# Optimization experiments

Hardware: AMD Instinct MI355X
Metric: run time of the kernel (lower is better)

Reference implementation:

```python
import jax, jax.numpy as jnp
import numpy as np
from jax import lax

NUM_TAGS = 64

def setup_inputs() -> dict:
    key = jax.random.key(0)
    ks = jax.random.split(key, 6)
    B, T, D, N = 64, 512, 1024, NUM_TAGS
    inputs = jax.random.normal(ks[0], (B, T, D), dtype=jnp.float32)
    mask = jnp.ones((B, T), dtype=jnp.int32)
    labels = jax.random.randint(ks[1], (B, T), 0, N)
    W = jax.random.normal(ks[2], (D, N), dtype=jnp.float32) / np.sqrt(D).astype(np.float32)
    b = jnp.zeros((N,), dtype=jnp.float32)
    transitions = jax.random.normal(ks[3], (N, N), dtype=jnp.float32) * 0.1
    start_transitions = jax.random.normal(ks[4], (N,), dtype=jnp.float32) * 0.1
    end_transitions = jax.random.normal(ks[5], (N,), dtype=jnp.float32) * 0.1
    return dict(inputs=inputs, mask=mask, labels=labels, W=W, b=b,
                transitions=transitions, start_transitions=start_transitions,
                end_transitions=end_transitions)


def _log_partition(logits, mask, trans, start, end):
    # forward algorithm (log-sum-exp recurrence). logits [B,T,N], mask bool [B,T]
    alpha = start[None, :] + logits[:, 0]                      # [B,N]
    emits = jnp.swapaxes(logits, 0, 1)[1:]                     # [T-1,B,N]
    ms = jnp.swapaxes(mask, 0, 1)[1:, :, None]                 # [T-1,B,1]
    def step(alpha, xs):
        emit, m = xs
        inner = alpha[:, :, None] + trans[None] + emit[:, None, :]  # [B,from,to]
        new = jax.nn.logsumexp(inner, axis=1)
        return jnp.where(m, new, alpha), None
    alpha, _ = lax.scan(step, alpha, (emits, ms))
    return jax.nn.logsumexp(alpha + end[None, :], axis=-1)     # [B]


def _joint_score(logits, tags, mask, trans, start, end):
    # score of the gold tag sequence (AllenNLP _joint_likelihood), vectorized
    maskf = mask.astype(logits.dtype)
    score = start[tags[:, 0]]
    score = score + jnp.sum(trans[tags[:, :-1], tags[:, 1:]] * maskf[:, 1:], axis=1)
    emit = jnp.take_along_axis(logits, tags[:, :, None], axis=2)[:, :, 0]   # [B,T]
    score = score + jnp.sum(emit * maskf, axis=1)
    last_idx = jnp.sum(mask.astype(jnp.int32), axis=1) - 1
    last_tags = jnp.take_along_axis(tags, last_idx[:, None], axis=1)[:, 0]
    return score + end[last_tags]


def _viterbi(logits, mask, trans, start, end):
    # batched Viterbi decode with backpointers; masked steps carry state through
    B, T, N = logits.shape
    alpha = start[None, :] + logits[:, 0]
    emits = jnp.swapaxes(logits, 0, 1)[1:]
    ms = jnp.swapaxes(mask, 0, 1)[1:, :, None]
    ident = jnp.broadcast_to(jnp.arange(N, dtype=jnp.int32)[None, :], (B, N))
    def step(alpha, xs):
        emit, m = xs
        sc = alpha[:, :, None] + trans[None] + emit[:, None, :]  # [B,from,to]
        best = jnp.max(sc, axis=1)
        bp = jnp.argmax(sc, axis=1).astype(jnp.int32)
        return jnp.where(m, best, alpha), jnp.where(m, bp, ident)
    alpha, bps = lax.scan(step, alpha, (emits, ms))
    last_tag = jnp.argmax(alpha + end[None, :], axis=-1).astype(jnp.int32)
    def back(tag, bp):
        prev = jnp.take_along_axis(bp, tag[:, None], axis=1)[:, 0]
        return prev, tag
    first, rest = lax.scan(back, last_tag, bps, reverse=True)
    tags = jnp.concatenate([first[None], rest], axis=0)          # [T,B]
    return jnp.swapaxes(tags, 0, 1) * mask.astype(jnp.int32)     # zero out padding


def reference(inputs, mask, labels, W, b, transitions, start_transitions, end_transitions):
    bool_mask = mask.astype(bool)
    logits = inputs @ W + b                                      # tag projection [B,T,N]
    scores = logits * mask[..., None].astype(logits.dtype)       # scores = inputs * mask
    tags = _viterbi(scores, bool_mask, transitions, start_transitions, end_transitions)
    log_z = _log_partition(scores, bool_mask, transitions, start_transitions, end_transitions)
    gold = _joint_score(scores, labels, bool_mask, transitions, start_transitions, end_transitions)
    loss = jnp.mean(log_z - gold)                                # mean negative log-likelihood
    return scores, tags, loss
```

## Files before the change

### kernel.cpp

```cpp
#include <hip/hip_runtime.h>
#include <cstdint>
#include <cstddef>

#define BB 64
#define TT 512
#define DD 1024
#define NTAG 64
#define CUT 255
#define SCORES_ELEMS (BB * TT * NTAG)
#define TAGS_OFF SCORES_ELEMS
#define LOSS_OFF (SCORES_ELEMS + BB * TT)

typedef __attribute__((ext_vector_type(8))) short short8;
typedef __attribute__((ext_vector_type(4))) float floatx4;
typedef __attribute__((ext_vector_type(16))) float f32x16;

__device__ __forceinline__ unsigned short f2bf_rne(float x) {
  const unsigned int u = __float_as_uint(x);
  const unsigned int r = u + 0x7FFFu + ((u >> 16) & 1u);
  return (unsigned short)(r >> 16);
}
__device__ __forceinline__ float bf2f(unsigned short h) {
  return __uint_as_float(((unsigned int)h) << 16);
}

__device__ __forceinline__ void block_sync_lds() {
  asm volatile("s_waitcnt lgkmcnt(0)\n\ts_barrier" ::: "memory");
}

__device__ __forceinline__ float quad_xor1(float v) {
  int x = __builtin_amdgcn_update_dpp(__float_as_int(v), __float_as_int(v), 0xB1, 0xf, 0xf, false);
  return __int_as_float(x);
}
__device__ __forceinline__ float quad_xor2(float v) {
  int x = __builtin_amdgcn_update_dpp(__float_as_int(v), __float_as_int(v), 0x4E, 0xf, 0xf, false);
  return __int_as_float(x);
}

__device__ __forceinline__ float dpp_red_max(float v) {
  int x;
  x = __builtin_amdgcn_update_dpp(__float_as_int(v), __float_as_int(v), 0x111, 0xf, 0xf, false);
  v = fmaxf(v, __int_as_float(x));
  x = __builtin_amdgcn_update_dpp(__float_as_int(v), __float_as_int(v), 0x112, 0xf, 0xf, false);
  v = fmaxf(v, __int_as_float(x));
  x = __builtin_amdgcn_update_dpp(__float_as_int(v), __float_as_int(v), 0x114, 0xf, 0xf, false);
  v = fmaxf(v, __int_as_float(x));
  x = __builtin_amdgcn_update_dpp(__float_as_int(v), __float_as_int(v), 0x118, 0xf, 0xf, false);
  v = fmaxf(v, __int_as_float(x));
  x = __builtin_amdgcn_update_dpp(__float_as_int(v), __float_as_int(v), 0x142, 0xa, 0xf, false);
  v = fmaxf(v, __int_as_float(x));
  x = __builtin_amdgcn_update_dpp(__float_as_int(v), __float_as_int(v), 0x143, 0xc, 0xf, false);
  v = fmaxf(v, __int_as_float(x));
  return __int_as_float(__builtin_amdgcn_readlane(__float_as_int(v), 63));
}

__device__ __forceinline__ float dpp_red_sum(float v) {
  int x;
  x = __builtin_amdgcn_update_dpp(__float_as_int(v), __float_as_int(v), 0x111, 0xf, 0xf, false);
  v = v + __int_as_float(x);
  x = __builtin_amdgcn_update_dpp(__float_as_int(v), __float_as_int(v), 0x112, 0xf, 0xf, false);
  v = v + __int_as_float(x);
  x = __builtin_amdgcn_update_dpp(__float_as_int(v), __float_as_int(v), 0x114, 0xf, 0xf, false);
  v = v + __int_as_float(x);
  x = __builtin_amdgcn_update_dpp(__float_as_int(v), __float_as_int(v), 0x118, 0xf, 0xf, false);
  v = v + __int_as_float(x);
  x = __builtin_amdgcn_update_dpp(__float_as_int(v), __float_as_int(v), 0x142, 0xa, 0xf, false);
  v = v + __int_as_float(x);
  x = __builtin_amdgcn_update_dpp(__float_as_int(v), __float_as_int(v), 0x143, 0xc, 0xf, false);
  v = v + __int_as_float(x);
  return __int_as_float(__builtin_amdgcn_readlane(__float_as_int(v), 63));
}

__global__ __launch_bounds__(256) void prep_w(
    const float* __restrict__ W, unsigned short* __restrict__ wf_hi,
    unsigned short* __restrict__ wf_lo) {
  const int f = blockIdx.x * 256 + threadIdx.x;
  const int kk = f >> 8;
  const int nt = (f >> 6) & 3;
  const int l = f & 63;
  const int n = nt * 16 + (l & 15);
  const int k0 = kk * 32 + ((l >> 4) << 3);
  short8 hv, lv;
#pragma unroll
  for (int j = 0; j < 8; ++j) {
    const float x = W[(size_t)(k0 + j) * NTAG + n];
    const unsigned short h = f2bf_rne(x);
    hv[j] = (short)h;
    lv[j] = (short)f2bf_rne(x - bf2f(h));
  }
  *reinterpret_cast<short8*>(wf_hi + (size_t)f * 8) = hv;
  *reinterpret_cast<short8*>(wf_lo + (size_t)f * 8) = lv;
}

__global__ __launch_bounds__(256, 6) void gemm_scores(
    const float* __restrict__ X, const int* __restrict__ mask,
    const unsigned short* __restrict__ wf_hi,
    const unsigned short* __restrict__ wf_lo,
    const float* __restrict__ bias, float* __restrict__ scores) {
  __shared__ float red[3 * 64 * 17];
  const int tid = threadIdx.x;
  const int lane = tid & 63;
  const int wv = tid >> 6;
  const int row0 = blockIdx.x * 16;
  const int arow = row0 + (lane & 15);
  const int aq = (lane >> 4) << 3;
  const float* Ap = X + (size_t)arow * DD + wv * 256 + aq;

  floatx4 acc[4];
#pragma unroll
  for (int nt = 0; nt < 4; ++nt) acc[nt] = (floatx4)(0.f);

  float4 a0 = *reinterpret_cast<const float4*>(Ap);
  float4 a1 = *reinterpret_cast<const float4*>(Ap + 4);

#pragma unroll
  for (int kk = 0; kk < 8; ++kk) {
    short8 ah, al;
    {
      const float v[8] = {a0.x, a0.y, a0.z, a0.w, a1.x, a1.y, a1.z, a1.w};
#pragma unroll
      for (int e = 0; e < 8; ++e) {
        const unsigned short h = f2bf_rne(v[e]);
        ah[e] = (short)h;
        al[e] = (short)f2bf_rne(v[e] - bf2f(h));
      }
    }
    if (kk < 7) {
      a0 = *reinterpret_cast<const float4*>(Ap + (kk + 1) * 32);
      a1 = *reinterpret_cast<const float4*>(Ap + (kk + 1) * 32 + 4);
    }
    const int kkAbs = wv * 8 + kk;
    const size_t fbase = (size_t)kkAbs * 4 * 64 * 8;
#pragma unroll
    for (int nt = 0; nt < 4; ++nt) {
      const size_t off = fbase + ((size_t)nt * 64 + lane) * 8;
      const short8 bh = *reinterpret_cast<const short8*>(wf_hi + off);
      const short8 bl = *reinterpret_cast<const short8*>(wf_lo + off);
      acc[nt] = __builtin_amdgcn_mfma_f32_16x16x32_bf16(ah, bh, acc[nt], 0, 0, 0);
      acc[nt] = __builtin_amdgcn_mfma_f32_16x16x32_bf16(ah, bl, acc[nt], 0, 0, 0);
      acc[nt] = __builtin_amdgcn_mfma_f32_16x16x32_bf16(al, bh, acc[nt], 0, 0, 0);
    }
  }

  if (wv > 0) {
    float* dst = &red[((wv - 1) * 64 + lane) * 17];
#pragma unroll
    for (int nt = 0; nt < 4; ++nt)
#pragma unroll
      for (int r = 0; r < 4; ++r) dst[nt * 4 + r] = acc[nt][r];
  }
  __syncthreads();
  if (wv == 0) {
#pragma unroll
    for (int w = 0; w < 3; ++w) {
      const float* srcp = &red[(w * 64 + lane) * 17];
#pragma unroll
      for (int nt = 0; nt < 4; ++nt)
#pragma unroll
        for (int r = 0; r < 4; ++r) acc[nt][r] += srcp[nt * 4 + r];
    }
    const int colb = lane & 15;
    const int quad = lane >> 4;
#pragma unroll
    for (int r = 0; r < 4; ++r) {
      const int row = row0 + quad * 4 + r;
      const float mf = (float)mask[row];
#pragma unroll
      for (int nt = 0; nt < 4; ++nt) {
        const int col = nt * 16 + colb;
        scores[(size_t)row * 64 + col] = (acc[nt][r] + bias[col]) * mf;
      }
    }
  }
}

__global__ __launch_bounds__(256, 1) void crf_forward(
    const float* __restrict__ scores, const int* __restrict__ mask,
    const float* __restrict__ trans, const float* __restrict__ startv,
    const float* __restrict__ endv, float* __restrict__ ws_alpha,
    float* __restrict__ ws_beta, float* __restrict__ zAcut,
    float* __restrict__ bScut, float* __restrict__ bVcut,
    float* __restrict__ Ca, float* __restrict__ Cb) {
  __shared__ float zbuf[2][NTAG];
  __shared__ float part[4];
  const int tid = threadIdx.x;
  const int wv = tid >> 6;
  const int lane = tid & 63;
  const int q = lane & 3;
  const int jl = lane >> 2;
  const int j = wv * 16 + jl;
  const int role = blockIdx.x >> 6;
  const int b = blockIdx.x & 63;
  const float* sc = scores + (size_t)b * TT * NTAG;
  const int* maskb = mask + b * TT;

  if (role == 0) {
    f32x16 tc;
#pragma unroll
    for (int i2 = 0; i2 < 16; ++i2)
      tc[i2] = trans[(size_t)(16 * q + i2) * NTAG + j];

    float aj = startv[j] + sc[j];
    if (q == 0) zbuf[0][j] = aj;
    float* wsA = ws_alpha + (size_t)b * 256 * NTAG;

    float e0 = sc[1 * NTAG + j], e1 = sc[2 * NTAG + j];
    float e2 = sc[3 * NTAG + j], e3 = sc[4 * NTAG + j];
    int k0 = maskb[1], k1 = maskb[2], k2 = maskb[3], k3 = maskb[4];
    __syncthreads();

    int cur = 0;
    for (int t = 1; t <= CUT; ++t) {
      if (q == 0) wsA[(size_t)(t - 1) * NTAG + j] = aj;
      const float4 a0 = *reinterpret_cast<const float4*>(&zbuf[cur][q * 16 + 0]);
      const float4 a1 = *reinterpret_cast<const float4*>(&zbuf[cur][q * 16 + 4]);
      const float4 a2 = *reinterpret_cast<const float4*>(&zbuf[cur][q * 16 + 8]);
      const float4 a3 = *reinterpret_cast<const float4*>(&zbuf[cur][q * 16 + 12]);
      const float emit = e0;
      const int m = k0;
      const int tp = (t + 4 <= CUT) ? (t + 4) : CUT;
      e0 = e1; e1 = e2; e2 = e3;
      e3 = sc[(size_t)tp * NTAG + j];
      k0 = k1; k1 = k2; k2 = k3;
      k3 = maskb[tp];

      const float c0 = a0.x + tc[0],  c1 = a0.y + tc[1];
      const float c2 = a0.z + tc[2],  c3 = a0.w + tc[3];
      const float c4 = a1.x + tc[4],  c5 = a1.y + tc[5];
      const float c6 = a1.z + tc[6],  c7 = a1.w + tc[7];
      const float c8 = a2.x + tc[8],  c9 = a2.y + tc[9];
      const float cA = a2.z + tc[10], cB = a2.w + tc[11];
      const float cC = a3.x + tc[12], cD = a3.y + tc[13];
      const float cE = a3.z + tc[14], cF = a3.w + tc[15];
      const float h0 = fmaxf(fmaxf(c0, c1), fmaxf(c2, c3));
      const float h1 = fmaxf(fmaxf(c4, c5), fmaxf(c6, c7));
      const float h2 = fmaxf(fmaxf(c8, c9), fmaxf(cA, cB));
      const float h3 = fmaxf(fmaxf(cC, cD), fmaxf(cE, cF));
      float pm = fmaxf(fmaxf(h0, h1), fmaxf(h2, h3));
      pm = fmaxf(pm, quad_xor1(pm));
      pm = fmaxf(pm, quad_xor2(pm));

      aj = m ? (pm + emit) : aj;
      const int nxt = cur ^ 1;
      if (q == 0) zbuf[nxt][j] = aj;
      block_sync_lds();
      cur = nxt;
    }
    if (q == 0) wsA[(size_t)255 * NTAG + j] = aj;
  } else if (role == 1) {
    f32x16 ec;
#pragma unroll
    for (int i2 = 0; i2 < 16; ++i2)
      ec[i2] = expf(trans[(size_t)(16 * q + i2) * NTAG + j]);

    const float a0v = startv[j] + sc[j];
    const float wm = dpp_red_max(a0v);
    if (lane == 0) part[wv] = wm;
    __syncthreads();
    const float M0 = fmaxf(fmaxf(part[0], part[1]), fmaxf(part[2], part[3]));
    float zj = expf(a0v - M0);
    float C = M0;
    if (q == 0) zbuf[0][j] = zj;

    float e0 = sc[1 * NTAG + j], e1 = sc[2 * NTAG + j];
    float e2 = sc[3 * NTAG + j], e3 = sc[4 * NTAG + j];
    int k0 = maskb[1], k1 = maskb[2], k2 = maskb[3], k3 = maskb[4];
    float pe = expf(e0);
    __syncthreads();

    int cur = 0;
    for (int t = 1; t <= CUT; ++t) {
      const float4 z0 = *reinterpret_cast<const float4*>(&zbuf[cur][q * 16 + 0]);
      const float4 z1 = *reinterpret_cast<const float4*>(&zbuf[cur][q * 16 + 4]);
      const float4 z2 = *reinterpret_cast<const float4*>(&zbuf[cur][q * 16 + 8]);
      const float4 z3 = *reinterpret_cast<const float4*>(&zbuf[cur][q * 16 + 12]);
      const float pec = pe;
      const int m = k0;
      const int tp = (t + 4 <= CUT) ? (t + 4) : CUT;
      e0 = e1; e1 = e2; e2 = e3;
      e3 = sc[(size_t)tp * NTAG + j];
      k0 = k1; k1 = k2; k2 = k3;
      k3 = maskb[tp];
      pe = expf(e0);

      float s0 = z0.x * ec[0], s1 = z0.y * ec[1];
      float s2 = z0.z * ec[2], s3 = z0.w * ec[3];
      s0 = fmaf(z1.x, ec[4], s0);  s1 = fmaf(z1.y, ec[5], s1);
      s2 = fmaf(z1.z, ec[6], s2);  s3 = fmaf(z1.w, ec[7], s3);
      s0 = fmaf(z2.x, ec[8], s0);  s1 = fmaf(z2.y, ec[9], s1);
      s2 = fmaf(z2.z, ec[10], s2); s3 = fmaf(z2.w, ec[11], s3);
      s0 = fmaf(z3.x, ec[12], s0); s1 = fmaf(z3.y, ec[13], s1);
      s2 = fmaf(z3.z, ec[14], s2); s3 = fmaf(z3.w, ec[15], s3);
      float s = (s0 + s1) + (s2 + s3);
      s += quad_xor1(s);
      s += quad_xor2(s);

      zj = m ? (s * pec) : zj;

      if ((t & 7) == 0) {
        const float ws = dpp_red_sum(zj);
        if (lane == 0) part[wv] = ws;
        block_sync_lds();
        const float S4 = (part[0] + part[1]) + (part[2] + part[3]);
        const float r = __builtin_amdgcn_rcpf(S4);
        zj *= 4.0f * r;
        C += logf(S4) - 1.3862943611198906f;
      }

      const int nxt = cur ^ 1;
      if (q == 0) zbuf[nxt][j] = zj;
      block_sync_lds();
      cur = nxt;
    }
    if (q == 0) zAcut[b * NTAG + j] = zj;
    if (tid == 0) Ca[b] = C;
  } else if (role == 2) {
    f32x16 tc;
#pragma unroll
    for (int i2 = 0; i2 < 16; ++i2)
      tc[i2] = trans[(size_t)j * NTAG + 16 * q + i2];

    float bj = endv[j];
    float* wsB = ws_beta + (size_t)b * 256 * NTAG;
    if (q == 0) {
      wsB[(size_t)255 * NTAG + j] = bj;
      zbuf[0][j] = bj + sc[(size_t)511 * NTAG + j];
    }
    float e0 = sc[(size_t)510 * NTAG + j], e1 = sc[(size_t)509 * NTAG + j];
    float e2 = sc[(size_t)508 * NTAG + j], e3 = sc[(size_t)507 * NTAG + j];
    int k0 = maskb[511], k1 = maskb[510], k2 = maskb[509], k3 = maskb[508];
    __syncthreads();

    int cur = 0;
    for (int t = 511; t >= 257; --t) {
      const float4 a0 = *reinterpret_cast<const float4*>(&zbuf[cur][q * 16 + 0]);
      const float4 a1 = *reinterpret_cast<const float4*>(&zbuf[cur][q * 16 + 4]);
      const float4 a2 = *reinterpret_cast<const float4*>(&zbuf[cur][q * 16 + 8]);
      const float4 a3 = *reinterpret_cast<const float4*>(&zbuf[cur][q * 16 + 12]);
      const float emit = e0;
      const int m = k0;
      const int tpe = (t - 5 >= 0) ? (t - 5) : 0;
      const int tpk = (t - 4 >= 256) ? (t - 4) : 256;
      e0 = e1; e1 = e2; e2 = e3;
      e3 = sc[(size_t)tpe * NTAG + j];
      k0 = k1; k1 = k2; k2 = k3;
      k3 = maskb[tpk];

      const float c0 = a0.x + tc[0],  c1 = a0.y + tc[1];
      const float c2 = a0.z + tc[2],  c3 = a0.w + tc[3];
      const float c4 = a1.x + tc[4],  c5 = a1.y + tc[5];
      const float c6 = a1.z + tc[6],  c7 = a1.w + tc[7];
      const float c8 = a2.x + tc[8],  c9 = a2.y + tc[9];
      const float cA = a2.z + tc[10], cB = a2.w + tc[11];
      const float cC = a3.x + tc[12], cD = a3.y + tc[13];
      const float cE = a3.z + tc[14], cF = a3.w + tc[15];
      const float h0 = fmaxf(fmaxf(c0, c1), fmaxf(c2, c3));
      const float h1 = fmaxf(fmaxf(c4, c5), fmaxf(c6, c7));
      const float h2 = fmaxf(fmaxf(c8, c9), fmaxf(cA, cB));
      const float h3 = fmaxf(fmaxf(cC, cD), fmaxf(cE, cF));
      float pm = fmaxf(fmaxf(h0, h1), fmaxf(h2, h3));
      pm = fmaxf(pm, quad_xor1(pm));
      pm = fmaxf(pm, quad_xor2(pm));

      bj = m ? pm : bj;
      const int nxt = cur ^ 1;
      if (q == 0) {
        wsB[(size_t)(t - 1 - 256) * NTAG + j] = bj;
        zbuf[nxt][j] = bj + emit;
      }
      block_sync_lds();
      cur = nxt;
    }
    {
      const float4 a0 = *reinterpret_cast<const float4*>(&zbuf[cur][q * 16 + 0]);
      const float4 a1 = *reinterpret_cast<const float4*>(&zbuf[cur][q * 16 + 4]);
      const float4 a2 = *reinterpret_cast<const float4*>(&zbuf[cur][q * 16 + 8]);
      const float4 a3 = *reinterpret_cast<const float4*>(&zbuf[cur][q * 16 + 12]);
      const float c0 = a0.x + tc[0],  c1 = a0.y + tc[1];
      const float c2 = a0.z + tc[2],  c3 = a0.w + tc[3];
      const float c4 = a1.x + tc[4],  c5 = a1.y + tc[5];
      const float c6 = a1.z + tc[6],  c7 = a1.w + tc[7];
      const float c8 = a2.x + tc[8],  c9 = a2.y + tc[9];
      const float cA = a2.z + tc[10], cB = a2.w + tc[11];
      const float cC = a3.x + tc[12], cD = a3.y + tc[13];
      const float cE = a3.z + tc[14], cF = a3.w + tc[15];
      const float h0 = fmaxf(fmaxf(c0, c1), fmaxf(c2, c3));
      const float h1 = fmaxf(fmaxf(c4, c5), fmaxf(c6, c7));
      const float h2 = fmaxf(fmaxf(c8, c9), fmaxf(cA, cB));
      const float h3 = fmaxf(fmaxf(cC, cD), fmaxf(cE, cF));
      float pm = fmaxf(fmaxf(h0, h1), fmaxf(h2, h3));
      pm = fmaxf(pm, quad_xor1(pm));
      pm = fmaxf(pm, quad_xor2(pm));
      bj = k0 ? pm : bj;
      if (q == 0) bVcut[b * NTAG + j] = bj;
    }
  } else {
    f32x16 ec;
#pragma unroll
    for (int i2 = 0; i2 < 16; ++i2)
      ec[i2] = expf(trans[(size_t)j * NTAG + 16 * q + i2]);

    float bj = expf(endv[j]);
    float C = 0.f;
    if (q == 0) zbuf[0][j] = bj * expf(sc[(size_t)511 * NTAG + j]);
    float e0 = sc[(size_t)510 * NTAG + j], e1 = sc[(size_t)509 * NTAG + j];
    float e2 = sc[(size_t)508 * NTAG + j], e3 = sc[(size_t)507 * NTAG + j];
    int k0 = maskb[511], k1 = maskb[510], k2 = maskb[509], k3 = maskb[508];
    float pe = expf(e0);
    __syncthreads();

    int cur = 0;
    for (int t = 511; t >= 257; --t) {
      const float4 z0 = *reinterpret_cast<const float4*>(&zbuf[cur][q * 16 + 0]);
      const float4 z1 = *reinterpret_cast<const float4*>(&zbuf[cur][q * 16 + 4]);
      const float4 z2 = *reinterpret_cast<const float4*>(&zbuf[cur][q * 16 + 8]);
      const float4 z3 = *reinterpret_cast<const float4*>(&zbuf[cur][q * 16 + 12]);
      const float pec = pe;
      const int m = k0;
      const int tpe = (t - 5 >= 0) ? (t - 5) : 0;
      const int tpk = (t - 4 >= 256) ? (t - 4) : 256;
      e0 = e1; e1 = e2; e2 = e3;
      e3 = sc[(size_t)tpe * NTAG + j];
      k0 = k1; k1 = k2; k2 = k3;
      k3 = maskb[tpk];
      pe = expf(e0);

      float s0 = z0.x * ec[0], s1 = z0.y * ec[1];
      float s2 = z0.z * ec[2], s3 = z0.w * ec[3];
      s0 = fmaf(z1.x, ec[4], s0);  s1 = fmaf(z1.y, ec[5], s1);
      s2 = fmaf(z1.z, ec[6], s2);  s3 = fmaf(z1.w, ec[7], s3);
      s0 = fmaf(z2.x, ec[8], s0);  s1 = fmaf(z2.y, ec[9], s1);
      s2 = fmaf(z2.z, ec[10], s2); s3 = fmaf(z2.w, ec[11], s3);
      s0 = fmaf(z3.x, ec[12], s0); s1 = fmaf(z3.y, ec[13], s1);
      s2 = fmaf(z3.z, ec[14], s2); s3 = fmaf(z3.w, ec[15], s3);
      float s = (s0 + s1) + (s2 + s3);
      s += quad_xor1(s);
      s += quad_xor2(s);

      bj = m ? s : bj;

      if ((t & 7) == 0) {
        const float ws = dpp_red_sum(bj);
        if (lane == 0) part[wv] = ws;
        block_sync_lds();
        const float S4 = (part[0] + part[1]) + (part[2] + part[3]);
        const float r = __builtin_amdgcn_rcpf(S4);
        bj *= 4.0f * r;
        C += logf(S4) - 1.3862943611198906f;
      }

      const int nxt = cur ^ 1;
      if (q == 0) zbuf[nxt][j] = bj * pec;
      block_sync_lds();
      cur = nxt;
    }
    {
      const float4 z0 = *reinterpret_cast<const float4*>(&zbuf[cur][q * 16 + 0]);
      const float4 z1 = *reinterpret_cast<const float4*>(&zbuf[cur][q * 16 + 4]);
      const float4 z2 = *reinterpret_cast<const float4*>(&zbuf[cur][q * 16 + 8]);
      const float4 z3 = *reinterpret_cast<const float4*>(&zbuf[cur][q * 16 + 12]);
      float s0 = z0.x * ec[0], s1 = z0.y * ec[1];
      float s2 = z0.z * ec[2], s3 = z0.w * ec[3];
      s0 = fmaf(z1.x, ec[4], s0);  s1 = fmaf(z1.y, ec[5], s1);
      s2 = fmaf(z1.z, ec[6], s2);  s3 = fmaf(z1.w, ec[7], s3);
      s0 = fmaf(z2.x, ec[8], s0);  s1 = fmaf(z2.y, ec[9], s1);
      s2 = fmaf(z2.z, ec[10], s2); s3 = fmaf(z2.w, ec[11], s3);
      s0 = fmaf(z3.x, ec[12], s0); s1 = fmaf(z3.y, ec[13], s1);
      s2 = fmaf(z3.z, ec[14], s2); s3 = fmaf(z3.w, ec[15], s3);
      float s = (s0 + s1) + (s2 + s3);
      s += quad_xor1(s);
      s += quad_xor2(s);
      bj = k0 ? s : bj;
      if (q == 0) bScut[b * NTAG + j] = bj;
      if (tid == 0) Cb[b] = C;
    }
  }
}

__global__ __launch_bounds__(64, 1) void crf_combine(
    const float* __restrict__ scores, const int* __restrict__ mask,
    const int* __restrict__ labels, const float* __restrict__ trans,
    const float* __restrict__ startv, const float* __restrict__ endv,
    const float* __restrict__ ws_alpha, const float* __restrict__ bVcut,
    const float* __restrict__ zAcut, const float* __restrict__ bScut,
    const float* __restrict__ Ca, const float* __restrict__ Cb,
    int* __restrict__ ws_lasttag, float* __restrict__ ws_loss) {
  const int lane = threadIdx.x;
  const int b = blockIdx.x;
  const float* sc = scores + (size_t)b * TT * NTAG;
  const int* maskb = mask + b * TT;

  const float aV = ws_alpha[((size_t)b * 256 + 255) * NTAG + lane];
  const float fv = aV + bVcut[b * NTAG + lane];
  const float mx = dpp_red_max(fv);
  const int jstar = (int)__builtin_ctzll(__ballot(fv == mx));
  if (lane == 0) ws_lasttag[b] = jstar;

  const float S = dpp_red_sum(zAcut[b * NTAG + lane] * bScut[b * NTAG + lane]);
  const float log_z = logf(S) + Ca[b] + Cb[b];

  float g = 0.f, msumf = 0.f;
  for (int t = lane; t < TT; t += 64) {
    const int lab = labels[b * TT + t];
    const float mf = (float)maskb[t];
    msumf += mf;
    g += sc[(size_t)t * NTAG + lab] * mf;
    if (t >= 1) {
      const int labp = labels[b * TT + t - 1];
      g += trans[(size_t)labp * NTAG + lab] * mf;
    }
  }
  g = dpp_red_sum(g);
  const float msum = dpp_red_sum(msumf);
  const int last_idx = (int)msum - 1;
  g += startv[labels[b * TT]] + endv[labels[b * TT + last_idx]];
  if (lane == 0) ws_loss[b] = log_z - g;
}

__global__ __launch_bounds__(64, 1) void viterbi_bt(
    const float* __restrict__ ws_alpha, const float* __restrict__ ws_beta,
    const int* __restrict__ ws_lasttag, const int* __restrict__ mask,
    const float* __restrict__ scores, const float* __restrict__ trans,
    float* __restrict__ out_tags) {
  __shared__ float tP[NTAG * 65];
  __shared__ int mk[256];
  __shared__ unsigned char tagb[256];
  const int lane = threadIdx.x;
  const int role = blockIdx.x >> 6;
  const int b = blockIdx.x & 63;

#pragma unroll
  for (int i = 0; i < NTAG; ++i) tP[i * 65 + lane] = trans[(size_t)i * NTAG + lane];
  const int tbase = role * 256;
  for (int t = lane; t < 256; t += 64) mk[t] = mask[b * TT + tbase + t];
  __syncthreads();

  int jcur = ws_lasttag[b];

  if (role == 0) {
    const float* wsA = ws_alpha + (size_t)b * 256 * NTAG;
    if (lane == 0) tagb[255] = (unsigned char)jcur;

    float a0 = wsA[(size_t)254 * NTAG + lane];
    float a1 = wsA[(size_t)253 * NTAG + lane];
    float a2 = wsA[(size_t)252 * NTAG + lane];
    float a3 = wsA[(size_t)251 * NTAG + lane];

    for (int s = 254; s >= 0; --s) {
      const float ac = a0;
      a0 = a1; a1 = a2; a2 = a3;
      const int sp = (s >= 4) ? (s - 4) : 0;
      a3 = wsA[(size_t)sp * NTAG + lane];
      if (mk[s + 1]) {
        const float c = ac + tP[lane * 65 + jcur];
        const float cmx = dpp_red_max(c);
        jcur = (int)__builtin_ctzll(__ballot(c == cmx));
      }
      if (lane == 0) tagb[s] = (unsigned char)jcur;
    }
  } else {
    const float* wsB = ws_beta + (size_t)b * 256 * NTAG;
    const float* scb = scores + (size_t)b * TT * NTAG;
    float r0 = wsB[(size_t)0 * NTAG + lane], r1 = wsB[(size_t)1 * NTAG + lane];
    float r2 = wsB[(size_t)2 * NTAG + lane], r3 = wsB[(size_t)3 * NTAG + lane];
    float s0 = scb[(size_t)256 * NTAG + lane], s1 = scb[(size_t)257 * NTAG + lane];
    float s2 = scb[(size_t)258 * NTAG + lane], s3 = scb[(size_t)259 * NTAG + lane];

    for (int t = 256; t < TT; ++t) {
      const float bv = r0, sv = s0;
      const int tb = (t + 4 < TT) ? (t + 4) : (TT - 1);
      r0 = r1; r1 = r2; r2 = r3;
      r3 = wsB[(size_t)(tb - 256) * NTAG + lane];
      s0 = s1; s1 = s2; s2 = s3;
      s3 = scb[(size_t)tb * NTAG + lane];
      if (mk[t - 256]) {
        const float c = tP[jcur * 65 + lane] + sv + bv;
        const float cmx = dpp_red_max(c);
        jcur = (int)__builtin_ctzll(__ballot(c == cmx));
      }
      if (lane == 0) tagb[t - 256] = (unsigned char)jcur;
    }
  }
  __syncthreads();
  for (int t = lane; t < 256; t += 64)
    out_tags[b * TT + tbase + t] = (float)(mk[t] ? (int)tagb[t] : 0);
}

__global__ __launch_bounds__(64, 1) void loss_mean(const float* __restrict__ ws_loss,
                                                   float* __restrict__ out) {
  const float v = ws_loss[threadIdx.x];
  const float s = dpp_red_sum(v);
  if (threadIdx.x == 0) out[0] = s * (1.0f / 64.0f);
}

extern "C" void kernel_launch(void* const* d_in, const int* in_sizes, int n_in,
                              void* d_out, int out_size, void* d_ws, size_t ws_size,
                              hipStream_t stream) {
  const float* X = (const float*)d_in[0];
  const int* mask = (const int*)d_in[1];
  const int* labels = (const int*)d_in[2];
  const float* W = (const float*)d_in[3];
  const float* bias = (const float*)d_in[4];
  const float* trans = (const float*)d_in[5];
  const float* startv = (const float*)d_in[6];
  const float* endv = (const float*)d_in[7];

  float* out = (float*)d_out;
  float* scores = out;
  float* out_tags = out + TAGS_OFF;
  float* out_loss = out + LOSS_OFF;

  unsigned short* wf_hi = (unsigned short*)d_ws;
  unsigned short* wf_lo = wf_hi + 65536;
  float* ws_alpha = (float*)(wf_lo + 65536);
  float* ws_beta = ws_alpha + (size_t)BB * 256 * NTAG;
  float* zAcut = ws_beta + (size_t)BB * 256 * NTAG;
  float* bScut = zAcut + BB * NTAG;
  float* bVcut = bScut + BB * NTAG;
  float* Ca = bVcut + BB * NTAG;
  float* Cb = Ca + BB;
  int* ws_lasttag = (int*)(Cb + BB);
  float* ws_loss = (float*)(ws_lasttag + BB);

  prep_w<<<32, 256, 0, stream>>>(W, wf_hi, wf_lo);
  gemm_scores<<<2048, 256, 0, stream>>>(X, mask, wf_hi, wf_lo, bias, scores);
  crf_forward<<<256, 256, 0, stream>>>(scores, mask, trans, startv, endv,
                                       ws_alpha, ws_beta, zAcut, bScut, bVcut,
                                       Ca, Cb);
  crf_combine<<<64, 64, 0, stream>>>(scores, mask, labels, trans, startv, endv,
                                     ws_alpha, bVcut, zAcut, bScut, Ca, Cb,
                                     ws_lasttag, ws_loss);
  viterbi_bt<<<128, 64, 0, stream>>>(ws_alpha, ws_beta, ws_lasttag, mask,
                                     scores, trans, out_tags);
  loss_mean<<<1, 64, 0, stream>>>(ws_loss, out_loss);
}
```

Baseline: 388.8 us.

## Fuse Viterbi and logsumexp recurrences per direction; merge backtrack halves into one block

The crf_forward kernel previously ran four separate 256-thread blocks per sequence (max-plus forward, sum-product forward, max-plus backward, sum-product backward). Each direction now runs both recurrences in one block, sharing the emission prefetch, the mask loads and the per-step barrier, so the grid shrinks from 256 to 128 blocks. The two-role Viterbi backtrack is likewise merged into one block per sequence that runs both halves in the same loop, and it now computes the argmax tag at the cut itself, which removes that step from crf_combine. The aim is to halve the number of serial dependency chains and barriers, at the cost of more instructions per step on each chain and fewer parallel blocks on the GPU.

```diff
diff --git a/kernel.cpp b/kernel.cpp
--- a/kernel.cpp
+++ b/kernel.cpp
@@ -181,7 +181,8 @@
     float* __restrict__ ws_beta, float* __restrict__ zAcut,
     float* __restrict__ bScut, float* __restrict__ bVcut,
     float* __restrict__ Ca, float* __restrict__ Cb) {
-  __shared__ float zbuf[2][NTAG];
+  __shared__ float zbV[2][NTAG];
+  __shared__ float zbS[2][NTAG];
   __shared__ float part[4];
   const int tid = threadIdx.x;
   const int wv = tid >> 6;
@@ -189,78 +190,30 @@
   const int q = lane & 3;
   const int jl = lane >> 2;
   const int j = wv * 16 + jl;
-  const int role = blockIdx.x >> 6;
+  const int dir = blockIdx.x >> 6;
   const int b = blockIdx.x & 63;
   const float* sc = scores + (size_t)b * TT * NTAG;
   const int* maskb = mask + b * TT;
 
-  if (role == 0) {
-    f32x16 tc;
-#pragma unroll
-    for (int i2 = 0; i2 < 16; ++i2)
-      tc[i2] = trans[(size_t)(16 * q + i2) * NTAG + j];
-
-    float aj = startv[j] + sc[j];
-    if (q == 0) zbuf[0][j] = aj;
-    float* wsA = ws_alpha + (size_t)b * 256 * NTAG;
-
-    float e0 = sc[1 * NTAG + j], e1 = sc[2 * NTAG + j];
-    float e2 = sc[3 * NTAG + j], e3 = sc[4 * NTAG + j];
-    int k0 = maskb[1], k1 = maskb[2], k2 = maskb[3], k3 = maskb[4];
-    __syncthreads();
-
-    int cur = 0;
-    for (int t = 1; t <= CUT; ++t) {
-      if (q == 0) wsA[(size_t)(t - 1) * NTAG + j] = aj;
-      const float4 a0 = *reinterpret_cast<const float4*>(&zbuf[cur][q * 16 + 0]);
-      const float4 a1 = *reinterpret_cast<const float4*>(&zbuf[cur][q * 16 + 4]);
-      const float4 a2 = *reinterpret_cast<const float4*>(&zbuf[cur][q * 16 + 8]);
-      const float4 a3 = *reinterpret_cast<const float4*>(&zbuf[cur][q * 16 + 12]);
-      const float emit = e0;
-      const int m = k0;
-      const int tp = (t + 4 <= CUT) ? (t + 4) : CUT;
-      e0 = e1; e1 = e2; e2 = e3;
-      e3 = sc[(size_t)tp * NTAG + j];
-      k0 = k1; k1 = k2; k2 = k3;
-      k3 = maskb[tp];
-
-      const float c0 = a0.x + tc[0],  c1 = a0.y + tc[1];
-      const float c2 = a0.z + tc[2],  c3 = a0.w + tc[3];
-      const float c4 = a1.x + tc[4],  c5 = a1.y + tc[5];
-      const float c6 = a1.z + tc[6],  c7 = a1.w + tc[7];
-      const float c8 = a2.x + tc[8],  c9 = a2.y + tc[9];
-      const float cA = a2.z + tc[10], cB = a2.w + tc[11];
-      const float cC = a3.x + tc[12], cD = a3.y + tc[13];
-      const float cE = a3.z + tc[14], cF = a3.w + tc[15];
-      const float h0 = fmaxf(fmaxf(c0, c1), fmaxf(c2, c3));
-      const float h1 = fmaxf(fmaxf(c4, c5), fmaxf(c6, c7));
-      const float h2 = fmaxf(fmaxf(c8, c9), fmaxf(cA, cB));
-      const float h3 = fmaxf(fmaxf(cC, cD), fmaxf(cE, cF));
-      float pm = fmaxf(fmaxf(h0, h1), fmaxf(h2, h3));
-      pm = fmaxf(pm, quad_xor1(pm));
-      pm = fmaxf(pm, quad_xor2(pm));
-
-      aj = m ? (pm + emit) : aj;
-      const int nxt = cur ^ 1;
-      if (q == 0) zbuf[nxt][j] = aj;
-      block_sync_lds();
-      cur = nxt;
-    }
-    if (q == 0) wsA[(size_t)255 * NTAG + j] = aj;
-  } else if (role == 1) {
-    f32x16 ec;
-#pragma unroll
-    for (int i2 = 0; i2 < 16; ++i2)
-      ec[i2] = expf(trans[(size_t)(16 * q + i2) * NTAG + j]);
+  if (dir == 0) {
+    f32x16 tc, ec;
+#pragma unroll
+    for (int i2 = 0; i2 < 16; ++i2) {
+      const float tv = trans[(size_t)(16 * q + i2) * NTAG + j];
+      tc[i2] = tv;
+      ec[i2] = expf(tv);
+    }
 
     const float a0v = startv[j] + sc[j];
+    float ajV = a0v;
     const float wm = dpp_red_max(a0v);
     if (lane == 0) part[wv] = wm;
     __syncthreads();
     const float M0 = fmaxf(fmaxf(part[0], part[1]), fmaxf(part[2], part[3]));
-    float zj = expf(a0v - M0);
+    float zjS = expf(a0v - M0);
     float C = M0;
-    if (q == 0) zbuf[0][j] = zj;
+    if (q == 0) { zbV[0][j] = ajV; zbS[0][j] = zjS; }
+    float* wsA = ws_alpha + (size_t)b * 256 * NTAG;
 
     float e0 = sc[1 * NTAG + j], e1 = sc[2 * NTAG + j];
     float e2 = sc[3 * NTAG + j], e3 = sc[4 * NTAG + j];
@@ -270,10 +223,16 @@
 
     int cur = 0;
     for (int t = 1; t <= CUT; ++t) {
-      const float4 z0 = *reinterpret_cast<const float4*>(&zbuf[cur][q * 16 + 0]);
-      const float4 z1 = *reinterpret_cast<const float4*>(&zbuf[cur][q * 16 + 4]);
-      const float4 z2 = *reinterpret_cast<const float4*>(&zbuf[cur][q * 16 + 8]);
-      const float4 z3 = *reinterpret_cast<const float4*>(&zbuf[cur][q * 16 + 12]);
+      if (q == 0) wsA[(size_t)(t - 1) * NTAG + j] = ajV;
+      const float4 v0 = *reinterpret_cast<const float4*>(&zbV[cur][q * 16 + 0]);
+      const float4 v1 = *reinterpret_cast<const float4*>(&zbV[cur][q * 16 + 4]);
+      const float4 v2 = *reinterpret_cast<const float4*>(&zbV[cur][q * 16 + 8]);
+      const float4 v3 = *reinterpret_cast<const float4*>(&zbV[cur][q * 16 + 12]);
+      const float4 z0 = *reinterpret_cast<const float4*>(&zbS[cur][q * 16 + 0]);
+      const float4 z1 = *reinterpret_cast<const float4*>(&zbS[cur][q * 16 + 4]);
+      const float4 z2 = *reinterpret_cast<const float4*>(&zbS[cur][q * 16 + 8]);
+      const float4 z3 = *reinterpret_cast<const float4*>(&zbS[cur][q * 16 + 12]);
+      const float emit = e0;
       const float pec = pe;
       const int m = k0;
       const int tp = (t + 4 <= CUT) ? (t + 4) : CUT;
@@ -282,6 +241,23 @@
       k0 = k1; k1 = k2; k2 = k3;
       k3 = maskb[tp];
       pe = expf(e0);
+
+      const float c0 = v0.x + tc[0],  c1 = v0.y + tc[1];
+      const float c2 = v0.z + tc[2],  c3 = v0.w + tc[3];
+      const float c4 = v1.x + tc[4],  c5 = v1.y + tc[5];
+      const float c6 = v1.z + tc[6],  c7 = v1.w + tc[7];
+      const float c8 = v2.x + tc[8],  c9 = v2.y + tc[9];
+      const float cA = v2.z + tc[10], cB = v2.w + tc[11];
+      const float cC = v3.x + tc[12], cD = v3.y + tc[13];
+      const float cE = v3.z + tc[14], cF = v3.w + tc[15];
+      const float h0 = fmaxf(fmaxf(c0, c1), fmaxf(c2, c3));
+      const float h1 = fmaxf(fmaxf(c4, c5), fmaxf(c6, c7));
+      const float h2 = fmaxf(fmaxf(c8, c9), fmaxf(cA, cB));
+      const float h3 = fmaxf(fmaxf(cC, cD), fmaxf(cE, cF));
+      float pm = fmaxf(fmaxf(h0, h1), fmaxf(h2, h3));
+      pm = fmaxf(pm, quad_xor1(pm));
+      pm = fmaxf(pm, quad_xor2(pm));
+      ajV = m ? (pm + emit) : ajV;
 
       float s0 = z0.x * ec[0], s1 = z0.y * ec[1];
       float s2 = z0.z * ec[2], s3 = z0.w * ec[3];
@@ -294,66 +270,84 @@
       float s = (s0 + s1) + (s2 + s3);
       s += quad_xor1(s);
       s += quad_xor2(s);
-
-      zj = m ? (s * pec) : zj;
+      zjS = m ? (s * pec) : zjS;
 
       if ((t & 7) == 0) {
-        const float ws = dpp_red_sum(zj);
+        const float ws = dpp_red_sum(zjS);
         if (lane == 0) part[wv] = ws;
         block_sync_lds();
         const float S4 = (part[0] + part[1]) + (part[2] + part[3]);
         const float r = __builtin_amdgcn_rcpf(S4);
-        zj *= 4.0f * r;
+        zjS *= 4.0f * r;
         C += logf(S4) - 1.3862943611198906f;
       }
 
       const int nxt = cur ^ 1;
-      if (q == 0) zbuf[nxt][j] = zj;
+      if (q == 0) { zbV[nxt][j] = ajV; zbS[nxt][j] = zjS; }
       block_sync_lds();
       cur = nxt;
     }
-    if (q == 0) zAcut[b * NTAG + j] = zj;
+    if (q == 0) {
+      wsA[(size_t)255 * NTAG + j] = ajV;
+      zAcut[b * NTAG + j] = zjS;
+    }
     if (tid == 0) Ca[b] = C;
-  } else if (role == 2) {
-    f32x16 tc;
-#pragma unroll
-    for (int i2 = 0; i2 < 16; ++i2)
-      tc[i2] = trans[(size_t)j * NTAG + 16 * q + i2];
-
-    float bj = endv[j];
+  } else {
+    f32x16 tc, ec;
+#pragma unroll
+    for (int i2 = 0; i2 < 16; ++i2) {
+      const float tv = trans[(size_t)j * NTAG + 16 * q + i2];
+      tc[i2] = tv;
+      ec[i2] = expf(tv);
+    }
+
+    float bjV = endv[j];
+    float bjS = expf(endv[j]);
+    float C = 0.f;
     float* wsB = ws_beta + (size_t)b * 256 * NTAG;
-    if (q == 0) {
-      wsB[(size_t)255 * NTAG + j] = bj;
-      zbuf[0][j] = bj + sc[(size_t)511 * NTAG + j];
+    {
+      const float e511 = sc[(size_t)511 * NTAG + j];
+      if (q == 0) {
+        wsB[(size_t)255 * NTAG + j] = bjV;
+        zbV[0][j] = bjV + e511;
+        zbS[0][j] = bjS * expf(e511);
+      }
     }
     float e0 = sc[(size_t)510 * NTAG + j], e1 = sc[(size_t)509 * NTAG + j];
     float e2 = sc[(size_t)508 * NTAG + j], e3 = sc[(size_t)507 * NTAG + j];
     int k0 = maskb[511], k1 = maskb[510], k2 = maskb[509], k3 = maskb[508];
+    float pe = expf(e0);
     __syncthreads();
 
     int cur = 0;
     for (int t = 511; t >= 257; --t) {
-      const float4 a0 = *reinterpret_cast<const float4*>(&zbuf[cur][q * 16 + 0]);
-      const float4 a1 = *reinterpret_cast<const float4*>(&zbuf[cur][q * 16 + 4]);
-      const float4 a2 = *reinterpret_cast<const float4*>(&zbuf[cur][q * 16 + 8]);
-      const float4 a3 = *reinterpret_cast<const float4*>(&zbuf[cur][q * 16 + 12]);
+      const float4 v0 = *reinterpret_cast<const float4*>(&zbV[cur][q * 16 + 0]);
+      const float4 v1 = *reinterpret_cast<const float4*>(&zbV[cur][q * 16 + 4]);
+      const float4 v2 = *reinterpret_cast<const float4*>(&zbV[cur][q * 16 + 8]);
+      const float4 v3 = *reinterpret_cast<const float4*>(&zbV[cur][q * 16 + 12]);
+      const float4 z0 = *reinterpret_cast<const float4*>(&zbS[cur][q * 16 + 0]);
+      const float4 z1 = *reinterpret_cast<const float4*>(&zbS[cur][q * 16 + 4]);
+      const float4 z2 = *reinterpret_cast<const float4*>(&zbS[cur][q * 16 + 8]);
+      const float4 z3 = *reinterpret_cast<const float4*>(&zbS[cur][q * 16 + 12]);
       const float emit = e0;
+      const float pec = pe;
       const int m = k0;
-      const int tpe = (t - 5 >= 0) ? (t - 5) : 0;
+      const int tpe = t - 5;
       const int tpk = (t - 4 >= 256) ? (t - 4) : 256;
       e0 = e1; e1 = e2; e2 = e3;
       e3 = sc[(size_t)tpe * NTAG + j];
       k0 = k1; k1 = k2; k2 = k3;
       k3 = maskb[tpk];
-
-      const float c0 = a0.x + tc[0],  c1 = a0.y + tc[1];
-      const float c2 = a0.z + tc[2],  c3 = a0.w + tc[3];
-      const float c4 = a1.x + tc[4],  c5 = a1.y + tc[5];
-      const float c6 = a1.z + tc[6],  c7 = a1.w + tc[7];
-      const float c8 = a2.x + tc[8],  c9 = a2.y + tc[9];
-      const float cA = a2.z + tc[10], cB = a2.w + tc[11];
-      const float cC = a3.x + tc[12], cD = a3.y + tc[13];
-      const float cE = a3.z + tc[14], cF = a3.w + tc[15];
+      pe = expf(e0);
+
+      const float c0 = v0.x + tc[0],  c1 = v0.y + tc[1];
+      const float c2 = v0.z + tc[2],  c3 = v0.w + tc[3];
+      const float c4 = v1.x + tc[4],  c5 = v1.y + tc[5];
+      const float c6 = v1.z + tc[6],  c7 = v1.w + tc[7];
+      const float c8 = v2.x + tc[8],  c9 = v2.y + tc[9];
+      const float cA = v2.z + tc[10], cB = v2.w + tc[11];
+      const float cC = v3.x + tc[12], cD = v3.y + tc[13];
+      const float cE = v3.z + tc[14], cF = v3.w + tc[15];
       const float h0 = fmaxf(fmaxf(c0, c1), fmaxf(c2, c3));
       const float h1 = fmaxf(fmaxf(c4, c5), fmaxf(c6, c7));
       const float h2 = fmaxf(fmaxf(c8, c9), fmaxf(cA, cB));
@@ -361,69 +355,7 @@
       float pm = fmaxf(fmaxf(h0, h1), fmaxf(h2, h3));
       pm = fmaxf(pm, quad_xor1(pm));
       pm = fmaxf(pm, quad_xor2(pm));
-
-      bj = m ? pm : bj;
-      const int nxt = cur ^ 1;
-      if (q == 0) {
-        wsB[(size_t)(t - 1 - 256) * NTAG + j] = bj;
-        zbuf[nxt][j] = bj + emit;
-      }
-      block_sync_lds();
-      cur = nxt;
-    }
-    {
-      const float4 a0 = *reinterpret_cast<const float4*>(&zbuf[cur][q * 16 + 0]);
-      const float4 a1 = *reinterpret_cast<const float4*>(&zbuf[cur][q * 16 + 4]);
-      const float4 a2 = *reinterpret_cast<const float4*>(&zbuf[cur][q * 16 + 8]);
-      const float4 a3 = *reinterpret_cast<const float4*>(&zbuf[cur][q * 16 + 12]);
-      const float c0 = a0.x + tc[0],  c1 = a0.y + tc[1];
-      const float c2 = a0.z + tc[2],  c3 = a0.w + tc[3];
-      const float c4 = a1.x + tc[4],  c5 = a1.y + tc[5];
-      const float c6 = a1.z + tc[6],  c7 = a1.w + tc[7];
-      const float c8 = a2.x + tc[8],  c9 = a2.y + tc[9];
-      const float cA = a2.z + tc[10], cB = a2.w + tc[11];
-      const float cC = a3.x + tc[12], cD = a3.y + tc[13];
-      const float cE = a3.z + tc[14], cF = a3.w + tc[15];
-      const float h0 = fmaxf(fmaxf(c0, c1), fmaxf(c2, c3));
-      const float h1 = fmaxf(fmaxf(c4, c5), fmaxf(c6, c7));
-      const float h2 = fmaxf(fmaxf(c8, c9), fmaxf(cA, cB));
-      const float h3 = fmaxf(fmaxf(cC, cD), fmaxf(cE, cF));
-      float pm = fmaxf(fmaxf(h0, h1), fmaxf(h2, h3));
-      pm = fmaxf(pm, quad_xor1(pm));
-      pm = fmaxf(pm, quad_xor2(pm));
-      bj = k0 ? pm : bj;
-      if (q == 0) bVcut[b * NTAG + j] = bj;
-    }
-  } else {
-    f32x16 ec;
-#pragma unroll
-    for (int i2 = 0; i2 < 16; ++i2)
-      ec[i2] = expf(trans[(size_t)j * NTAG + 16 * q + i2]);
-
-    float bj = expf(endv[j]);
-    float C = 0.f;
-    if (q == 0) zbuf[0][j] = bj * expf(sc[(size_t)511 * NTAG + j]);
-    float e0 = sc[(size_t)510 * NTAG + j], e1 = sc[(size_t)509 * NTAG + j];
-    float e2 = sc[(size_t)508 * NTAG + j], e3 = sc[(size_t)507 * NTAG + j];
-    int k0 = maskb[511], k1 = maskb[510], k2 = maskb[509], k3 = maskb[508];
-    float pe = expf(e0);
-    __syncthreads();
-
-    int cur = 0;
-    for (int t = 511; t >= 257; --t) {
-      const float4 z0 = *reinterpret_cast<const float4*>(&zbuf[cur][q * 16 + 0]);
-      const float4 z1 = *reinterpret_cast<const float4*>(&zbuf[cur][q * 16 + 4]);
-      const float4 z2 = *reinterpret_cast<const float4*>(&zbuf[cur][q * 16 + 8]);
-      const float4 z3 = *reinterpret_cast<const float4*>(&zbuf[cur][q * 16 + 12]);
-      const float pec = pe;
-      const int m = k0;
-      const int tpe = (t - 5 >= 0) ? (t - 5) : 0;
-      const int tpk = (t - 4 >= 256) ? (t - 4) : 256;
-      e0 = e1; e1 = e2; e2 = e3;
-      e3 = sc[(size_t)tpe * NTAG + j];
-      k0 = k1; k1 = k2; k2 = k3;
-      k3 = maskb[tpk];
-      pe = expf(e0);
+      bjV = m ? pm : bjV;
 
       float s0 = z0.x * ec[0], s1 = z0.y * ec[1];
       float s2 = z0.z * ec[2], s3 = z0.w * ec[3];
@@ -436,29 +368,53 @@
       float s = (s0 + s1) + (s2 + s3);
       s += quad_xor1(s);
       s += quad_xor2(s);
-
-      bj = m ? s : bj;
+      bjS = m ? s : bjS;
 
       if ((t & 7) == 0) {
-        const float ws = dpp_red_sum(bj);
+        const float ws = dpp_red_sum(bjS);
         if (lane == 0) part[wv] = ws;
         block_sync_lds();
         const float S4 = (part[0] + part[1]) + (part[2] + part[3]);
         const float r = __builtin_amdgcn_rcpf(S4);
-        bj *= 4.0f * r;
+        bjS *= 4.0f * r;
         C += logf(S4) - 1.3862943611198906f;
       }
 
       const int nxt = cur ^ 1;
-      if (q == 0) zbuf[nxt][j] = bj * pec;
+      if (q == 0) {
+        wsB[(size_t)(t - 257) * NTAG + j] = bjV;
+        zbV[nxt][j] = bjV + emit;
+        zbS[nxt][j] = bjS * pec;
+      }
       block_sync_lds();
       cur = nxt;
     }
     {
-      const float4 z0 = *reinterpret_cast<const float4*>(&zbuf[cur][q * 16 + 0]);
-      const float4 z1 = *reinterpret_cast<const float4*>(&zbuf[cur][q * 16 + 4]);
-      const float4 z2 = *reinterpret_cast<const float4*>(&zbuf[cur][q * 16 + 8]);
-      const float4 z3 = *reinterpret_cast<const float4*>(&zbuf[cur][q * 16 + 12]);
+      const float4 v0 = *reinterpret_cast<const float4*>(&zbV[cur][q * 16 + 0]);
+      const float4 v1 = *reinterpret_cast<const float4*>(&zbV[cur][q * 16 + 4]);
+      const float4 v2 = *reinterpret_cast<const float4*>(&zbV[cur][q * 16 + 8]);
+      const float4 v3 = *reinterpret_cast<const float4*>(&zbV[cur][q * 16 + 12]);
+      const float4 z0 = *reinterpret_cast<const float4*>(&zbS[cur][q * 16 + 0]);
+      const float4 z1 = *reinterpret_cast<const float4*>(&zbS[cur][q * 16 + 4]);
+      const float4 z2 = *reinterpret_cast<const float4*>(&zbS[cur][q * 16 + 8]);
+      const float4 z3 = *reinterpret_cast<const float4*>(&zbS[cur][q * 16 + 12]);
+      const float c0 = v0.x + tc[0],  c1 = v0.y + tc[1];
+      const float c2 = v0.z + tc[2],  c3 = v0.w + tc[3];
+      const float c4 = v1.x + tc[4],  c5 = v1.y + tc[5];
+      const float c6 = v1.z + tc[6],  c7 = v1.w + tc[7];
+      const float c8 = v2.x + tc[8],  c9 = v2.y + tc[9];
+      const float cA = v2.z + tc[10], cB = v2.w + tc[11];
+      const float cC = v3.x + tc[12], cD = v3.y + tc[13];
+      const float cE = v3.z + tc[14], cF = v3.w + tc[15];
+      const float h0 = fmaxf(fmaxf(c0, c1), fmaxf(c2, c3));
+      const float h1 = fmaxf(fmaxf(c4, c5), fmaxf(c6, c7));
+      const float h2 = fmaxf(fmaxf(c8, c9), fmaxf(cA, cB));
+      const float h3 = fmaxf(fmaxf(cC, cD), fmaxf(cE, cF));
+      float pm = fmaxf(fmaxf(h0, h1), fmaxf(h2, h3));
+      pm = fmaxf(pm, quad_xor1(pm));
+      pm = fmaxf(pm, quad_xor2(pm));
+      bjV = k0 ? pm : bjV;
+
       float s0 = z0.x * ec[0], s1 = z0.y * ec[1];
       float s2 = z0.z * ec[2], s3 = z0.w * ec[3];
       s0 = fmaf(z1.x, ec[4], s0);  s1 = fmaf(z1.y, ec[5], s1);
@@ -470,8 +426,9 @@
       float s = (s0 + s1) + (s2 + s3);
       s += quad_xor1(s);
       s += quad_xor2(s);
-      bj = k0 ? s : bj;
-      if (q == 0) bScut[b * NTAG + j] = bj;
+      bjS = k0 ? s : bjS;
+
+      if (q == 0) { bVcut[b * NTAG + j] = bjV; bScut[b * NTAG + j] = bjS; }
       if (tid == 0) Cb[b] = C;
     }
   }
@@ -481,20 +438,13 @@
     const float* __restrict__ scores, const int* __restrict__ mask,
     const int* __restrict__ labels, const float* __restrict__ trans,
     const float* __restrict__ startv, const float* __restrict__ endv,
-    const float* __restrict__ ws_alpha, const float* __restrict__ bVcut,
     const float* __restrict__ zAcut, const float* __restrict__ bScut,
     const float* __restrict__ Ca, const float* __restrict__ Cb,
-    int* __restrict__ ws_lasttag, float* __restrict__ ws_loss) {
+    float* __restrict__ ws_loss) {
   const int lane = threadIdx.x;
   const int b = blockIdx.x;
   const float* sc = scores + (size_t)b * TT * NTAG;
   const int* maskb = mask + b * TT;
-
-  const float aV = ws_alpha[((size_t)b * 256 + 255) * NTAG + lane];
-  const float fv = aV + bVcut[b * NTAG + lane];
-  const float mx = dpp_red_max(fv);
-  const int jstar = (int)__builtin_ctzll(__ballot(fv == mx));
-  if (lane == 0) ws_lasttag[b] = jstar;
 
   const float S = dpp_red_sum(zAcut[b * NTAG + lane] * bScut[b * NTAG + lane]);
   const float log_z = logf(S) + Ca[b] + Cb[b];
@@ -519,71 +469,84 @@
 
 __global__ __launch_bounds__(64, 1) void viterbi_bt(
     const float* __restrict__ ws_alpha, const float* __restrict__ ws_beta,
-    const int* __restrict__ ws_lasttag, const int* __restrict__ mask,
+    const float* __restrict__ bVcut, const int* __restrict__ mask,
     const float* __restrict__ scores, const float* __restrict__ trans,
     float* __restrict__ out_tags) {
   __shared__ float tP[NTAG * 65];
-  __shared__ int mk[256];
-  __shared__ unsigned char tagb[256];
+  __shared__ int mk[TT];
+  __shared__ unsigned char tagbP[256];
+  __shared__ unsigned char tagbS[256];
   const int lane = threadIdx.x;
-  const int role = blockIdx.x >> 6;
-  const int b = blockIdx.x & 63;
+  const int b = blockIdx.x;
 
 #pragma unroll
   for (int i = 0; i < NTAG; ++i) tP[i * 65 + lane] = trans[(size_t)i * NTAG + lane];
-  const int tbase = role * 256;
-  for (int t = lane; t < 256; t += 64) mk[t] = mask[b * TT + tbase + t];
-  __syncthreads();
-
-  int jcur = ws_lasttag[b];
-
-  if (role == 0) {
-    const float* wsA = ws_alpha + (size_t)b * 256 * NTAG;
-    if (lane == 0) tagb[255] = (unsigned char)jcur;
-
-    float a0 = wsA[(size_t)254 * NTAG + lane];
-    float a1 = wsA[(size_t)253 * NTAG + lane];
-    float a2 = wsA[(size_t)252 * NTAG + lane];
-    float a3 = wsA[(size_t)251 * NTAG + lane];
-
-    for (int s = 254; s >= 0; --s) {
-      const float ac = a0;
-      a0 = a1; a1 = a2; a2 = a3;
-      const int sp = (s >= 4) ? (s - 4) : 0;
-      a3 = wsA[(size_t)sp * NTAG + lane];
-      if (mk[s + 1]) {
-        const float c = ac + tP[lane * 65 + jcur];
-        const float cmx = dpp_red_max(c);
-        jcur = (int)__builtin_ctzll(__ballot(c == cmx));
-      }
-      if (lane == 0) tagb[s] = (unsigned char)jcur;
-    }
-  } else {
-    const float* wsB = ws_beta + (size_t)b * 256 * NTAG;
-    const float* scb = scores + (size_t)b * TT * NTAG;
-    float r0 = wsB[(size_t)0 * NTAG + lane], r1 = wsB[(size_t)1 * NTAG + lane];
-    float r2 = wsB[(size_t)2 * NTAG + lane], r3 = wsB[(size_t)3 * NTAG + lane];
-    float s0 = scb[(size_t)256 * NTAG + lane], s1 = scb[(size_t)257 * NTAG + lane];
-    float s2 = scb[(size_t)258 * NTAG + lane], s3 = scb[(size_t)259 * NTAG + lane];
-
-    for (int t = 256; t < TT; ++t) {
-      const float bv = r0, sv = s0;
-      const int tb = (t + 4 < TT) ? (t + 4) : (TT - 1);
-      r0 = r1; r1 = r2; r2 = r3;
-      r3 = wsB[(size_t)(tb - 256) * NTAG + lane];
-      s0 = s1; s1 = s2; s2 = s3;
-      s3 = scb[(size_t)tb * NTAG + lane];
-      if (mk[t - 256]) {
-        const float c = tP[jcur * 65 + lane] + sv + bv;
-        const float cmx = dpp_red_max(c);
-        jcur = (int)__builtin_ctzll(__ballot(c == cmx));
-      }
-      if (lane == 0) tagb[t - 256] = (unsigned char)jcur;
-    }
-  }
-  __syncthreads();
-  for (int t = lane; t < 256; t += 64)
-    out_tags[b * TT + tbase + t] = (float)(mk[t] ? (int)tagb[t] : 0);
+  for (int t = lane; t < TT; t += 64) mk[t] = mask[b * TT + t];
+
+  const float* wsA = ws_alpha + (size_t)b * 256 * NTAG;
+  const float* wsB = ws_beta + (size_t)b * 256 * NTAG;
+  const float* scb = scores + (size_t)b * TT * NTAG;
+
+  const float fv = wsA[(size_t)255 * NTAG + lane] + bVcut[b * NTAG + lane];
+  const float mx = dpp_red_max(fv);
+  int jP = (int)__builtin_ctzll(__ballot(fv == mx));
+  int jS = jP;
+  if (lane == 0) tagbP[255] = (unsigned char)jP;
+
+  float a0 = wsA[(size_t)254 * NTAG + lane];
+  float a1 = wsA[(size_t)253 * NTAG + lane];
+  float a2 = wsA[(size_t)252 * NTAG + lane];
+  float a3 = wsA[(size_t)251 * NTAG + lane];
+  float r0 = wsB[(size_t)0 * NTAG + lane], r1 = wsB[(size_t)1 * NTAG + lane];
+  float r2 = wsB[(size_t)2 * NTAG + lane], r3 = wsB[(size_t)3 * NTAG + lane];
+  float s0 = scb[(size_t)256 * NTAG + lane], s1 = scb[(size_t)257 * NTAG + lane];
+  float s2 = scb[(size_t)258 * NTAG + lane], s3 = scb[(size_t)259 * NTAG + lane];
+
+  {
+    const float bv = r0, sv = s0;
+    r0 = r1; r1 = r2; r2 = r3; r3 = wsB[(size_t)4 * NTAG + lane];
+    s0 = s1; s1 = s2; s2 = s3; s3 = scb[(size_t)260 * NTAG + lane];
+    if (mk[256]) {
+      const float c = tP[jS * 65 + lane] + sv + bv;
+      const float cmx = dpp_red_max(c);
+      jS = (int)__builtin_ctzll(__ballot(c == cmx));
+    }
+    if (lane == 0) tagbS[0] = (unsigned char)jS;
+  }
+
+  for (int i = 0; i < 255; ++i) {
+    const int s = 254 - i;
+    const int t = 257 + i;
+    const float ac = a0;
+    a0 = a1; a1 = a2; a2 = a3;
+    const int sp = (s >= 4) ? (s - 4) : 0;
+    a3 = wsA[(size_t)sp * NTAG + lane];
+    const float bv = r0, sv = s0;
+    const int tb = (t + 4 < TT) ? (t + 4) : (TT - 1);
+    r0 = r1; r1 = r2; r2 = r3; r3 = wsB[(size_t)(tb - 256) * NTAG + lane];
+    s0 = s1; s1 = s2; s2 = s3; s3 = scb[(size_t)tb * NTAG + lane];
+    const float tpP = tP[lane * 65 + jP];
+    const float tpS = tP[jS * 65 + lane];
+    if (mk[s + 1]) {
+      const float c = ac + tpP;
+      const float cmx = dpp_red_max(c);
+      jP = (int)__builtin_ctzll(__ballot(c == cmx));
+    }
+    if (mk[t]) {
+      const float c = tpS + sv + bv;
+      const float cmx = dpp_red_max(c);
+      jS = (int)__builtin_ctzll(__ballot(c == cmx));
+    }
+    if (lane == 0) {
+      tagbP[s] = (unsigned char)jP;
+      tagbS[t - 256] = (unsigned char)jS;
+    }
+  }
+
+  for (int t = lane; t < TT; t += 64) {
+    const int tag = (t < 256) ? (int)tagbP[t] : (int)tagbS[t - 256];
+    out_tags[b * TT + t] = (float)(mk[t] ? tag : 0);
+  }
 }
 
 __global__ __launch_bounds__(64, 1) void loss_mean(const float* __restrict__ ws_loss,
@@ -619,18 +582,16 @@
   float* bVcut = bScut + BB * NTAG;
   float* Ca = bVcut + BB * NTAG;
   float* Cb = Ca + BB;
-  int* ws_lasttag = (int*)(Cb + BB);
-  float* ws_loss = (float*)(ws_lasttag + BB);
+  float* ws_loss = Cb + BB;
 
   prep_w<<<32, 256, 0, stream>>>(W, wf_hi, wf_lo);
   gemm_scores<<<2048, 256, 0, stream>>>(X, mask, wf_hi, wf_lo, bias, scores);
-  crf_forward<<<256, 256, 0, stream>>>(scores, mask, trans, startv, endv,
+  crf_forward<<<128, 256, 0, stream>>>(scores, mask, trans, startv, endv,
                                        ws_alpha, ws_beta, zAcut, bScut, bVcut,
                                        Ca, Cb);
+  viterbi_bt<<<64, 64, 0, stream>>>(ws_alpha, ws_beta, bVcut, mask,
+                                    scores, trans, out_tags);
   crf_combine<<<64, 64, 0, stream>>>(scores, mask, labels, trans, startv, endv,
-                                     ws_alpha, bVcut, zAcut, bScut, Ca, Cb,
-                                     ws_lasttag, ws_loss);
-  viterbi_bt<<<128, 64, 0, stream>>>(ws_alpha, ws_beta, ws_lasttag, mask,
-                                     scores, trans, out_tags);
+                                     zAcut, bScut, Ca, Cb, ws_loss);
   loss_mean<<<1, 64, 0, stream>>>(ws_loss, out_loss);
 }
```

Result: slower. 466.5 us (+20.0%).
